# Kernel tuning notes

Measured on AMD Instinct MI355X. Metric: run time of the kernel, lower is better.

Reference implementation:

```python
import jax, jax.numpy as jnp
import numpy as np

B, S, E = 2, 2048, 1024
H, NQ = 16, 8          # n_heads, n_qubits
D = E // H             # head_dim


def setup_inputs() -> dict:
    key = jax.random.key(0)
    ks = jax.random.split(key, 11)
    sc = 0.02
    return {
        "query": jax.random.normal(ks[0], (B, S, E), jnp.float32),
        "key":   jax.random.normal(ks[1], (B, S, E), jnp.float32),
        "value": jax.random.normal(ks[2], (B, S, E), jnp.float32),
        "Wq": jax.random.normal(ks[3], (E, NQ), jnp.float32) * sc,
        "bq": jnp.zeros((NQ,), jnp.float32),
        "Wk": jax.random.normal(ks[4], (E, NQ), jnp.float32) * sc,
        "bk": jnp.zeros((NQ,), jnp.float32),
        "Wv": jax.random.normal(ks[5], (E, E), jnp.float32) * sc,
        "bv": jnp.zeros((E,), jnp.float32),
        "Wo": jax.random.normal(ks[6], (E, E), jnp.float32) * sc,
        "bo": jnp.zeros((E,), jnp.float32),
    }


def reference(query, key, value, Wq, bq, Wk, bk, Wv, bv, Wo, bo):
    # Linear encoders (q/k are computed in the original but, because
    # _apply_rotation is the identity, they never influence the scores).
    q = query @ Wq + bq            # [B,S,NQ] (dead math, kept for fidelity)
    k = key @ Wk + bk              # [B,S,NQ]
    v = value @ Wv + bv            # [B,S,E]
    v = v.reshape(B, S, H, D).transpose(0, 2, 1, 3)  # [B,H,S,D]

    # Quantum overlap: both encoded states are always |0>, so
    # |<q_state|k_state>|^2 == 1 for every (b,i,j) pair.
    scores = jnp.full((B, H, S, S), 1.0 / np.sqrt(NQ), dtype=query.dtype)
    attn = jax.nn.softmax(scores, axis=-1)           # uniform 1/S weights

    out = jnp.einsum('bhij,bhjd->bhid', attn, v)     # [B,H,S,D]
    out = out.transpose(0, 2, 1, 3).reshape(B, S, E)
    out = out @ Wo + bo
    return out, attn
```

## Files before the change

kernel.cpp:

```cpp
#include <hip/hip_runtime.h>


typedef float floatx4 __attribute__((ext_vector_type(4)));

#define ATTN_BASE4 1048576LL
#define CHUNK4     8388608LL
#define FILLB      2048

__device__ __forceinline__ void fill_chunk(float* __restrict__ out,
                                           int fb, long long chunk_base) {
    floatx4* o4 = (floatx4*)out;
    const floatx4 av = (floatx4)(1.0f / 2048.0f);
    long long base = chunk_base + (long long)fb * 4096 + threadIdx.x;
    #pragma unroll
    for (int it = 0; it < 16; ++it)
        __builtin_nontemporal_store(av, &o4[base + it * 256]);
}

__global__ void k1_colsum_fill(const float* __restrict__ value,
                               float* __restrict__ part1,
                               float* __restrict__ out) {
    int blk = blockIdx.x;
    if (blk < 256) {
        int b  = blk >> 7, sp = blk & 127, tid = threadIdx.x;
        const floatx4* v4 = (const floatx4*)value;
        floatx4 acc = (floatx4)0.0f;
        int rowbase = b * 2048 + sp * 16;
        #pragma unroll
        for (int r = 0; r < 16; ++r)
            acc += v4[(size_t)(rowbase + r) * 256 + tid];
        ((floatx4*)part1)[(size_t)(b * 128 + sp) * 256 + tid] = acc;
    } else {
        fill_chunk(out, blk - 256, ATTN_BASE4 + 0 * CHUNK4);
    }
}

__global__ void k2_mv1_fill(const float* __restrict__ part1,
                            const float* __restrict__ Wv,
                            float* __restrict__ t1p,
                            float* __restrict__ out) {
    int blk = blockIdx.x;
    if (blk < 64) {
        __shared__ float red[256];
        __shared__ float vbar[32];
        int t = threadIdx.x;
        int b = blk >> 5, ks = blk & 31, k0 = ks * 32;
        int kl = t >> 3, seg = t & 7;
        float s = 0.f;
        #pragma unroll
        for (int i = 0; i < 16; ++i) {
            int sp = seg * 16 + i;
            s += part1[(size_t)(b * 128 + sp) * 1024 + k0 + kl];
        }
        red[t] = s;
        __syncthreads();
        if (t < 32) {
            float v = 0.f;
            #pragma unroll
            for (int j = 0; j < 8; ++j) v += red[t * 8 + j];
            vbar[t] = v * (1.0f / 2048.0f);
        }
        __syncthreads();
        const floatx4* W4 = (const floatx4*)Wv;
        floatx4 acc = (floatx4)0.0f;
        #pragma unroll 8
        for (int kk = 0; kk < 32; ++kk)
            acc += vbar[kk] * W4[(size_t)(k0 + kk) * 256 + t];
        ((floatx4*)t1p)[(size_t)(b * 32 + ks) * 256 + t] = acc;
    } else {
        fill_chunk(out, blk - 64, ATTN_BASE4 + 1 * CHUNK4);
    }
}

__global__ void k3_mv2_fill(const float* __restrict__ t1p,
                            const float* __restrict__ bv,
                            const float* __restrict__ Wo,
                            float* __restrict__ t2p,
                            float* __restrict__ out) {
    int blk = blockIdx.x;
    if (blk < 64) {
        __shared__ float red[256];
        __shared__ float vbar2[32];
        int t = threadIdx.x;
        int b = blk >> 5, ks = blk & 31, k0 = ks * 32;
        int kl = t >> 3, seg = t & 7;
        float s = 0.f;
        #pragma unroll
        for (int i = 0; i < 4; ++i) {
            int sp = seg * 4 + i;
            s += t1p[(size_t)(b * 32 + sp) * 1024 + k0 + kl];
        }
        red[t] = s;
        __syncthreads();
        if (t < 32) {
            float v = bv[k0 + t];
            #pragma unroll
            for (int j = 0; j < 8; ++j) v += red[t * 8 + j];
            vbar2[t] = v;
        }
        __syncthreads();
        const floatx4* W4 = (const floatx4*)Wo;
        floatx4 acc = (floatx4)0.0f;
        #pragma unroll 8
        for (int kk = 0; kk < 32; ++kk)
            acc += vbar2[kk] * W4[(size_t)(k0 + kk) * 256 + t];
        ((floatx4*)t2p)[(size_t)(b * 32 + ks) * 256 + t] = acc;
    } else {
        fill_chunk(out, blk - 64, ATTN_BASE4 + 2 * CHUNK4);
    }
}

__global__ void k4_bcast_fill(const float* __restrict__ t2p,
                              const float* __restrict__ bo,
                              float* __restrict__ out) {
    int blk = blockIdx.x;
    if (blk < 64) {
        __shared__ __align__(16) float orow[1024];
        int t = threadIdx.x;
        int b = blk >> 5, rg = blk & 31;
        int r0 = rg * 64;
        #pragma unroll
        for (int cc = 0; cc < 4; ++cc) {
            int col = cc * 256 + t;
            float s = bo[col];
            for (int sp = 0; sp < 32; ++sp)
                s += t2p[(size_t)(b * 32 + sp) * 1024 + col];
            orow[col] = s;
        }
        __syncthreads();
        floatx4 w = ((const floatx4*)orow)[t];
        floatx4* o4 = (floatx4*)out;
        size_t rowbase = ((size_t)b * 2048 + r0) * 256;
        #pragma unroll 4
        for (int r = 0; r < 64; ++r)
            __builtin_nontemporal_store(w, &o4[rowbase + (size_t)r * 256 + t]);
    } else {
        fill_chunk(out, blk - 64, ATTN_BASE4 + 3 * CHUNK4);
    }
}

extern "C" void kernel_launch(void* const* d_in, const int* in_sizes, int n_in,
                              void* d_out, int out_size, void* d_ws, size_t ws_size,
                              hipStream_t stream) {
    const float* value = (const float*)d_in[2];
    const float* Wv    = (const float*)d_in[7];
    const float* bv    = (const float*)d_in[8];
    const float* Wo    = (const float*)d_in[9];
    const float* bo    = (const float*)d_in[10];
    float* out = (float*)d_out;

    float* ws    = (float*)d_ws;
    float* part1 = ws;
    float* t1p   = part1 + 262144;
    float* t2p   = t1p   + 65536;

    k1_colsum_fill<<<256 + FILLB, 256, 0, stream>>>(value, part1, out);
    k2_mv1_fill   <<< 64 + FILLB, 256, 0, stream>>>(part1, Wv, t1p, out);
    k3_mv2_fill   <<< 64 + FILLB, 256, 0, stream>>>(t1p, bv, Wo, t2p, out);
    k4_bcast_fill <<< 64 + FILLB, 256, 0, stream>>>(t2p, bo, out);
}
```

Baseline: 109.0 us.

## Fold Wv and Wo into one matrix and merge pipeline into two kernels

Computes the combined weight Wv@Wo (plus folded bias bv@Wo+bo) in the first kernel alongside the column sums of value and part of the attention fill. A second kernel then does one matrix-vector product with the combined weight and broadcasts the output rows while finishing the fill. This removes two kernel launches and their serialization, but adds a full 1024^3 GEMM of extra arithmetic per call that must hide behind the bandwidth-bound fill. A fallback four-kernel path remains if workspace is too small.

```diff
diff --git a/kernel.cpp b/kernel.cpp
--- a/kernel.cpp
+++ b/kernel.cpp
@@ -4,25 +4,125 @@
 typedef float floatx4 __attribute__((ext_vector_type(4)));
 
 #define ATTN_BASE4 1048576LL
-#define CHUNK4     8388608LL
-#define FILLB      2048
-
-__device__ __forceinline__ void fill_chunk(float* __restrict__ out,
-                                           int fb, long long chunk_base) {
+#define TOT4       34603008LL
+#define K1_FILLB   3840
+#define K1_FILL4   15728640LL
+#define K2_FILLB   4352
+
+__device__ __forceinline__ void fill_at(float* __restrict__ out, long long f4base) {
     floatx4* o4 = (floatx4*)out;
     const floatx4 av = (floatx4)(1.0f / 2048.0f);
-    long long base = chunk_base + (long long)fb * 4096 + threadIdx.x;
+    long long base = f4base + threadIdx.x;
     #pragma unroll
     for (int it = 0; it < 16; ++it)
         __builtin_nontemporal_store(av, &o4[base + it * 256]);
 }
 
-__global__ void k1_colsum_fill(const float* __restrict__ value,
-                               float* __restrict__ part1,
-                               float* __restrict__ out) {
-    int blk = blockIdx.x;
+__global__ void __launch_bounds__(256)
+k1_colsum_gemm_fill(const float* __restrict__ value,
+                    const float* __restrict__ Wv, const float* __restrict__ bv,
+                    const float* __restrict__ Wo, const float* __restrict__ bo,
+                    float* __restrict__ part1, float* __restrict__ wc,
+                    float* __restrict__ out) {
+    int blk = blockIdx.x, t = threadIdx.x;
     if (blk < 256) {
-        int b  = blk >> 7, sp = blk & 127, tid = threadIdx.x;
+        int b = blk >> 7, sp = blk & 127;
+        const floatx4* v4 = (const floatx4*)value;
+        floatx4 acc = (floatx4)0.0f;
+        int rowbase = b * 2048 + sp * 16;
+        #pragma unroll
+        for (int r = 0; r < 16; ++r)
+            acc += v4[(size_t)(rowbase + r) * 256 + t];
+        ((floatx4*)part1)[(size_t)(b * 128 + sp) * 256 + t] = acc;
+    } else if (blk < 528) {
+        int g = blk - 256;
+        int kt = g >> 4, et = g & 15;
+        int k_local = t >> 2, eq = t & 3;
+        int e0 = et * 64 + eq * 16;
+        const float* arow;
+        bool active = true;
+        if (kt < 16) arow = Wv + (size_t)(kt * 64 + k_local) * 1024;
+        else { active = (k_local == 0); arow = bv; }
+        if (active) {
+            const floatx4* W4 = (const floatx4*)Wo;
+            floatx4 a0 = (floatx4)0.f, a1 = (floatx4)0.f,
+                    a2 = (floatx4)0.f, a3 = (floatx4)0.f;
+            int c4 = e0 >> 2;
+            #pragma unroll 4
+            for (int j = 0; j < 1024; ++j) {
+                float s = arow[j];
+                const floatx4* wr = W4 + (size_t)j * 256 + c4;
+                a0 += s * wr[0]; a1 += s * wr[1];
+                a2 += s * wr[2]; a3 += s * wr[3];
+            }
+            floatx4* dst;
+            if (kt < 16) {
+                dst = (floatx4*)(wc + (size_t)(kt * 64 + k_local) * 1024 + e0);
+            } else {
+                const floatx4* b4 = (const floatx4*)bo;
+                a0 += b4[c4]; a1 += b4[c4 + 1]; a2 += b4[c4 + 2]; a3 += b4[c4 + 3];
+                dst = (floatx4*)(wc + (size_t)1024 * 1024 + e0);
+            }
+            dst[0] = a0; dst[1] = a1; dst[2] = a2; dst[3] = a3;
+        }
+    } else {
+        fill_at(out, ATTN_BASE4 + (long long)(blk - 528) * 4096);
+    }
+}
+
+__global__ void __launch_bounds__(256)
+k2_outrow_bcast_fill(const float* __restrict__ part1,
+                     const float* __restrict__ wc,
+                     float* __restrict__ out) {
+    int blk = blockIdx.x, t = threadIdx.x;
+    if (blk < 64) {
+        __shared__ __align__(16) float vbar[1024];
+        __shared__ float red[256];
+        __shared__ __align__(16) float orow[32];
+        int b = blk >> 5, es = blk & 31;
+        int e0 = es * 32;
+        const floatx4* p4 = (const floatx4*)part1 + (size_t)b * 128 * 256;
+        floatx4 acc = (floatx4)0.0f;
+        for (int sp = 0; sp < 128; ++sp)
+            acc += p4[sp * 256 + t];
+        ((floatx4*)vbar)[t] = acc * (1.0f / 2048.0f);
+        __syncthreads();
+        int es_l = t & 31, seg = t >> 5;
+        const float* wcol = wc + e0 + es_l;
+        float part = 0.f;
+        int kbase = seg * 128;
+        #pragma unroll 8
+        for (int kk = 0; kk < 128; ++kk) {
+            int k = kbase + kk;
+            part += vbar[k] * wcol[(size_t)k * 1024];
+        }
+        red[t] = part;
+        __syncthreads();
+        if (t < 32) {
+            float o = wc[(size_t)1024 * 1024 + e0 + t];
+            #pragma unroll
+            for (int g = 0; g < 8; ++g) o += red[g * 32 + t];
+            orow[t] = o;
+        }
+        __syncthreads();
+        floatx4 w = ((const floatx4*)orow)[t & 7];
+        int rg = t >> 3;
+        floatx4* o4 = (floatx4*)out;
+        size_t colbase = (size_t)es * 8 + (t & 7);
+        size_t rowstart = (size_t)b * 2048 + (size_t)rg * 64;
+        #pragma unroll 8
+        for (int i = 0; i < 64; ++i)
+            __builtin_nontemporal_store(w, &o4[(rowstart + i) * 256 + colbase]);
+    } else {
+        fill_at(out, ATTN_BASE4 + K1_FILL4 + (long long)(blk - 64) * 4096);
+    }
+}
+
+__global__ void fb_colsum_fill(const float* __restrict__ value,
+                               float* __restrict__ part1, float* __restrict__ out) {
+    int blk = blockIdx.x;
+    if (blk < 256) {
+        int b = blk >> 7, sp = blk & 127, tid = threadIdx.x;
         const floatx4* v4 = (const floatx4*)value;
         floatx4 acc = (floatx4)0.0f;
         int rowbase = b * 2048 + sp * 16;
@@ -30,95 +130,67 @@
         for (int r = 0; r < 16; ++r)
             acc += v4[(size_t)(rowbase + r) * 256 + tid];
         ((floatx4*)part1)[(size_t)(b * 128 + sp) * 256 + tid] = acc;
-    } else {
-        fill_chunk(out, blk - 256, ATTN_BASE4 + 0 * CHUNK4);
-    }
-}
-
-__global__ void k2_mv1_fill(const float* __restrict__ part1,
-                            const float* __restrict__ Wv,
-                            float* __restrict__ t1p,
-                            float* __restrict__ out) {
-    int blk = blockIdx.x;
-    if (blk < 64) {
-        __shared__ float red[256];
-        __shared__ float vbar[32];
-        int t = threadIdx.x;
-        int b = blk >> 5, ks = blk & 31, k0 = ks * 32;
+    } else fill_at(out, ATTN_BASE4 + 0 * 8388608LL + (long long)(blk - 256) * 4096);
+}
+__global__ void fb_mv1_fill(const float* __restrict__ part1, const float* __restrict__ Wv,
+                            float* __restrict__ t1p, float* __restrict__ out) {
+    int blk = blockIdx.x;
+    if (blk < 64) {
+        __shared__ float red[256]; __shared__ float vb[32];
+        int t = threadIdx.x, b = blk >> 5, ks = blk & 31, k0 = ks * 32;
         int kl = t >> 3, seg = t & 7;
         float s = 0.f;
         #pragma unroll
-        for (int i = 0; i < 16; ++i) {
-            int sp = seg * 16 + i;
-            s += part1[(size_t)(b * 128 + sp) * 1024 + k0 + kl];
-        }
-        red[t] = s;
-        __syncthreads();
+        for (int i = 0; i < 16; ++i)
+            s += part1[(size_t)(b * 128 + seg * 16 + i) * 1024 + k0 + kl];
+        red[t] = s; __syncthreads();
         if (t < 32) {
             float v = 0.f;
             #pragma unroll
             for (int j = 0; j < 8; ++j) v += red[t * 8 + j];
-            vbar[t] = v * (1.0f / 2048.0f);
+            vb[t] = v * (1.0f / 2048.0f);
         }
         __syncthreads();
         const floatx4* W4 = (const floatx4*)Wv;
         floatx4 acc = (floatx4)0.0f;
         #pragma unroll 8
-        for (int kk = 0; kk < 32; ++kk)
-            acc += vbar[kk] * W4[(size_t)(k0 + kk) * 256 + t];
+        for (int kk = 0; kk < 32; ++kk) acc += vb[kk] * W4[(size_t)(k0 + kk) * 256 + t];
         ((floatx4*)t1p)[(size_t)(b * 32 + ks) * 256 + t] = acc;
-    } else {
-        fill_chunk(out, blk - 64, ATTN_BASE4 + 1 * CHUNK4);
-    }
-}
-
-__global__ void k3_mv2_fill(const float* __restrict__ t1p,
-                            const float* __restrict__ bv,
+    } else fill_at(out, ATTN_BASE4 + 1 * 8388608LL + (long long)(blk - 64) * 4096);
+}
+__global__ void fb_mv2_fill(const float* __restrict__ t1p, const float* __restrict__ bv,
                             const float* __restrict__ Wo,
-                            float* __restrict__ t2p,
-                            float* __restrict__ out) {
-    int blk = blockIdx.x;
-    if (blk < 64) {
-        __shared__ float red[256];
-        __shared__ float vbar2[32];
-        int t = threadIdx.x;
-        int b = blk >> 5, ks = blk & 31, k0 = ks * 32;
+                            float* __restrict__ t2p, float* __restrict__ out) {
+    int blk = blockIdx.x;
+    if (blk < 64) {
+        __shared__ float red[256]; __shared__ float vb2[32];
+        int t = threadIdx.x, b = blk >> 5, ks = blk & 31, k0 = ks * 32;
         int kl = t >> 3, seg = t & 7;
         float s = 0.f;
         #pragma unroll
-        for (int i = 0; i < 4; ++i) {
-            int sp = seg * 4 + i;
-            s += t1p[(size_t)(b * 32 + sp) * 1024 + k0 + kl];
-        }
-        red[t] = s;
-        __syncthreads();
+        for (int i = 0; i < 4; ++i)
+            s += t1p[(size_t)(b * 32 + seg * 4 + i) * 1024 + k0 + kl];
+        red[t] = s; __syncthreads();
         if (t < 32) {
             float v = bv[k0 + t];
             #pragma unroll
             for (int j = 0; j < 8; ++j) v += red[t * 8 + j];
-            vbar2[t] = v;
+            vb2[t] = v;
         }
         __syncthreads();
         const floatx4* W4 = (const floatx4*)Wo;
         floatx4 acc = (floatx4)0.0f;
         #pragma unroll 8
-        for (int kk = 0; kk < 32; ++kk)
-            acc += vbar2[kk] * W4[(size_t)(k0 + kk) * 256 + t];
+        for (int kk = 0; kk < 32; ++kk) acc += vb2[kk] * W4[(size_t)(k0 + kk) * 256 + t];
         ((floatx4*)t2p)[(size_t)(b * 32 + ks) * 256 + t] = acc;
-    } else {
-        fill_chunk(out, blk - 64, ATTN_BASE4 + 2 * CHUNK4);
-    }
-}
-
-__global__ void k4_bcast_fill(const float* __restrict__ t2p,
-                              const float* __restrict__ bo,
+    } else fill_at(out, ATTN_BASE4 + 2 * 8388608LL + (long long)(blk - 64) * 4096);
+}
+__global__ void fb_bcast_fill(const float* __restrict__ t2p, const float* __restrict__ bo,
                               float* __restrict__ out) {
     int blk = blockIdx.x;
     if (blk < 64) {
         __shared__ __align__(16) float orow[1024];
-        int t = threadIdx.x;
-        int b = blk >> 5, rg = blk & 31;
-        int r0 = rg * 64;
+        int t = threadIdx.x, b = blk >> 5, rg = blk & 31;
         #pragma unroll
         for (int cc = 0; cc < 4; ++cc) {
             int col = cc * 256 + t;
@@ -130,13 +202,11 @@
         __syncthreads();
         floatx4 w = ((const floatx4*)orow)[t];
         floatx4* o4 = (floatx4*)out;
-        size_t rowbase = ((size_t)b * 2048 + r0) * 256;
+        size_t rowbase = ((size_t)b * 2048 + rg * 64) * 256;
         #pragma unroll 4
         for (int r = 0; r < 64; ++r)
             __builtin_nontemporal_store(w, &o4[rowbase + (size_t)r * 256 + t]);
-    } else {
-        fill_chunk(out, blk - 64, ATTN_BASE4 + 3 * CHUNK4);
-    }
+    } else fill_at(out, ATTN_BASE4 + 3 * 8388608LL + (long long)(blk - 64) * 4096);
 }
 
 extern "C" void kernel_launch(void* const* d_in, const int* in_sizes, int n_in,
@@ -148,14 +218,22 @@
     const float* Wo    = (const float*)d_in[9];
     const float* bo    = (const float*)d_in[10];
     float* out = (float*)d_out;
-
-    float* ws    = (float*)d_ws;
-    float* part1 = ws;
-    float* t1p   = part1 + 262144;
-    float* t2p   = t1p   + 65536;
-
-    k1_colsum_fill<<<256 + FILLB, 256, 0, stream>>>(value, part1, out);
-    k2_mv1_fill   <<< 64 + FILLB, 256, 0, stream>>>(part1, Wv, t1p, out);
-    k3_mv2_fill   <<< 64 + FILLB, 256, 0, stream>>>(t1p, bv, Wo, t2p, out);
-    k4_bcast_fill <<< 64 + FILLB, 256, 0, stream>>>(t2p, bo, out);
-}
+    float* ws  = (float*)d_ws;
+
+    const size_t need = (size_t)(262144 + 1025 * 1024 + 256) * 4;
+    if (ws_size >= need) {
+        float* part1 = ws;
+        float* wc    = ws + 262144;
+        k1_colsum_gemm_fill<<<256 + 272 + K1_FILLB, 256, 0, stream>>>(
+            value, Wv, bv, Wo, bo, part1, wc, out);
+        k2_outrow_bcast_fill<<<64 + K2_FILLB, 256, 0, stream>>>(part1, wc, out);
+    } else {
+        float* part1 = ws;
+        float* t1p   = ws + 262144;
+        float* t2p   = t1p + 65536;
+        fb_colsum_fill<<<256 + 2048, 256, 0, stream>>>(value, part1, out);
+        fb_mv1_fill   <<< 64 + 2048, 256, 0, stream>>>(part1, Wv, t1p, out);
+        fb_mv2_fill   <<< 64 + 2048, 256, 0, stream>>>(t1p, bv, Wo, t2p, out);
+        fb_bcast_fill <<< 64 + 2048, 256, 0, stream>>>(t2p, bo, out);
+    }
+}
```

Result: slower. 369.8 us (+239.4%).
